# Performance work log

Hardware: AMD Instinct MI355X
Metric: run time of the kernel (lower is better)

## Reference

```python
import jax, jax.numpy as jnp
import numpy as np

B, SP, SH, H = 32, 256, 256, 512
D = 2 * H       # input feature dim (2*hidden_size)
E = H // 2      # per-liner output dim
FD = 4 * H      # fusion linear dim
EPS = 1e-13


def setup_inputs() -> dict:
    key = jax.random.key(0)
    ks = jax.random.split(key, 8)
    s = 0.02
    return dict(
        premise_batch=jax.random.normal(ks[0], (B, SP, D), jnp.float32),
        hypothesis_batch=jax.random.normal(ks[1], (B, SH, D), jnp.float32),
        premise_mask=jax.random.randint(ks[2], (B, SP), 0, 2).astype(jnp.int32),
        hypothesis_mask=jax.random.randint(ks[3], (B, SH), 0, 2).astype(jnp.int32),
        W8=jax.random.normal(ks[4], (8, D, E), jnp.float32) * s,   # liner1..8 weights (in,out)
        B8=jnp.zeros((8, E), jnp.float32),
        Wl=jax.random.normal(ks[5], (8 * E, FD), jnp.float32) * s,  # self.liner
        bl=jnp.zeros((FD,), jnp.float32),
        Wp=jax.random.normal(ks[6], (7 * D, H), jnp.float32) * s,   # self._projection
        bp=jnp.zeros((H,), jnp.float32),
    )


def masked_softmax(logits, mask):
    # ESIM-style: multiply logits by mask, softmax, re-mask, renormalize.
    m = mask[:, None, :]                        # (b,1,kv)
    r = jax.nn.softmax(logits * m, axis=-1) * m
    return r / (r.sum(axis=-1, keepdims=True) + EPS)


def fuse(x, imp_self, imp_inter, W8, B8, Wl, bl):
    # x: (b,s,D); imp_*: (b,s,1). Eight modulated views -> liner1..8 -> concat -> liner+ReLU.
    a1 = imp_self * imp_inter
    a2 = imp_self + imp_inter
    a3 = jnp.maximum(imp_self, imp_inter)
    x1 = x * imp_self
    x2 = x * imp_inter
    mx = jnp.maximum(x1, x2)
    feats = jnp.stack([x * a1, x * a2, x * a3, mx,
                       x * (a1 + 1.0), x * (a2 + 1.0), x * (a3 + 1.0), mx + x], 0)  # (8,b,s,D)
    h = jnp.einsum('kbsd,kde->kbse', feats, W8) + B8[:, None, None, :]              # (8,b,s,E)
    cat = jnp.moveaxis(h, 0, 2).reshape(x.shape[0], x.shape[1], 8 * E)              # concat order 1..8
    return jax.nn.relu(cat @ Wl + bl)           # dropout is identity in eval mode


def reference(premise_batch, hypothesis_batch, premise_mask, hypothesis_mask,
              W8, B8, Wl, bl, Wp, bp):
    pm = premise_mask.astype(jnp.float32)
    hm = hypothesis_mask.astype(jnp.float32)
    scale = 1.0 / jnp.sqrt(jnp.float32(premise_batch.shape[-1]))

    sim = jnp.einsum('bpd,bhd->bph', premise_batch, hypothesis_batch) * scale
    ph = masked_softmax(sim, hm)                               # (b,Sp,Sh)
    hp = masked_softmax(sim.transpose(0, 2, 1), pm)            # (b,Sh,Sp)
    att_p = jnp.einsum('bph,bhd->bpd', ph, hypothesis_batch) * pm[:, :, None]
    att_h = jnp.einsum('bhp,bpd->bhd', hp, premise_batch) * hm[:, :, None]

    sp_attn = jax.nn.softmax(jnp.einsum('bpd,bqd->bpq', premise_batch, premise_batch) * scale, axis=-1)
    sh_attn = jax.nn.softmax(jnp.einsum('bpd,bqd->bpq', hypothesis_batch, hypothesis_batch) * scale, axis=-1)
    self_p = sp_attn @ premise_batch
    self_h = sh_attn @ hypothesis_batch

    imp_p = sp_attn.sum(axis=-2)[..., None]        # (b,Sp,1)
    imp_h = sh_attn.sum(axis=-2)[..., None]        # (b,Sh,1)
    inter_imp_h = ph.sum(axis=-2)[..., None]       # (b,Sh,1)
    inter_imp_p = hp.sum(axis=-2)[..., None]       # (b,Sp,1)

    p_all = fuse(premise_batch, imp_p, inter_imp_p, W8, B8, Wl, bl)
    h_all = fuse(hypothesis_batch, imp_h, inter_imp_h, W8, B8, Wl, bl)

    enh_p = jnp.concatenate([premise_batch, att_p, self_p, p_all,
                             premise_batch * att_p, premise_batch - att_p], axis=-1)
    enh_h = jnp.concatenate([hypothesis_batch, att_h, self_h, h_all,
                             hypothesis_batch * att_h, hypothesis_batch - att_h], axis=-1)
    out_p = jax.nn.relu(enh_p @ Wp + bp)
    out_h = jax.nn.relu(enh_h @ Wp + bp)
    return out_p, out_h
```

## Files before the change

### kernel.cpp

```cpp
#include <hip/hip_runtime.h>
#include <hip/hip_bf16.h>
#include <cmath>

#define BB 32
#define SS 256
#define DD 1024
#define EE 256
#define FDIM 2048
#define HH 512
#define KOUT6 (6 * 1024)
#define NROW (BB * SS)
#define NROW2 (2 * NROW)
#define SIMSZ ((size_t)BB * SS * SS)

static constexpr float SCALE = 1.0f / 32.0f;
static constexpr float EPSF  = 1e-13f;

typedef __attribute__((ext_vector_type(8))) short bf16x8;
typedef __attribute__((ext_vector_type(4))) float f32x4;

__device__ inline float4 ld4(const float* p) { return *(const float4*)p; }
__device__ inline ushort f2b(float f) {
    uint x = __float_as_uint(f);
    x += 0x7fffu + ((x >> 16) & 1u);
    return (ushort)(x >> 16);
}
__device__ inline float b2f(ushort u) { return __uint_as_float(((uint)u) << 16); }
__device__ inline bf16x8 cvt8(const float* v) {
    bf16x8 r;
#pragma unroll
    for (int j = 0; j < 8; ++j) r[j] = (short)f2b(v[j]);
    return r;
}
__device__ inline void b2f8(bf16x8 v, float* o) {
#pragma unroll
    for (int j = 0; j < 8; ++j) o[j] = b2f((ushort)v[j]);
}

typedef __attribute__((address_space(1))) const uchar gas_t;
typedef __attribute__((address_space(3))) uchar las_t;
__device__ inline void gll16(const ushort* g, ushort* l) {
    __builtin_amdgcn_global_load_lds((gas_t*)g, (las_t*)l, 16, 0, 0);
}

__device__ inline int swz_orig_2d() {
    const int n   = blockIdx.y * gridDim.x + blockIdx.x;
    const int tot = gridDim.x * gridDim.y;
    return (n & 7) * (tot >> 3) + (n >> 3);
}
__device__ inline int swz_orig_3d() {
    const int n   = (blockIdx.z * gridDim.y + blockIdx.y) * gridDim.x + blockIdx.x;
    const int tot = gridDim.x * gridDim.y * gridDim.z;
    return (n & 7) * (tot >> 3) + (n >> 3);
}

__global__ __launch_bounds__(256)
void tpose_cvt_k(const float* __restrict__ in, ushort* __restrict__ out,
                 int K, int N, size_t inStride, size_t outStride) {
    __shared__ float T[32][33];
    const float* ib = in  + (size_t)blockIdx.z * inStride;
    ushort*      ob = out + (size_t)blockIdx.z * outStride;
    const int k0 = blockIdx.x * 32, n0 = blockIdx.y * 32;
    const int tx = threadIdx.x & 31, ty = threadIdx.x >> 5;
#pragma unroll
    for (int i = 0; i < 4; ++i) T[ty + 8 * i][tx] = ib[(size_t)(k0 + ty + 8 * i) * N + n0 + tx];
    __syncthreads();
#pragma unroll
    for (int i = 0; i < 4; ++i)
        ob[(size_t)(n0 + ty + 8 * i) * K + k0 + tx] = f2b(T[tx][ty + 8 * i]);
}

__global__ __launch_bounds__(256)
void tpose_wp_k(const float* __restrict__ Wp, ushort* __restrict__ out) {
    __shared__ float T[32][33];
    const int k0 = blockIdx.x * 32, n0 = blockIdx.y * 32;
    const int tx = threadIdx.x & 31, ty = threadIdx.x >> 5;
#pragma unroll
    for (int i = 0; i < 4; ++i) {
        const int k = k0 + ty + 8 * i, n = n0 + tx;
        float v = Wp[(size_t)k * HH + n];
        if (k < DD)           v += Wp[(size_t)(k + 6 * DD) * HH + n];
        else if (k < 2 * DD)  v -= Wp[(size_t)(k + 5 * DD) * HH + n];
        T[ty + 8 * i][tx] = v;
    }
    __syncthreads();
#pragma unroll
    for (int i = 0; i < 4; ++i)
        out[(size_t)(n0 + ty + 8 * i) * KOUT6 + k0 + tx] = f2b(T[tx][ty + 8 * i]);
}

__global__ __launch_bounds__(256)
void cvt_xb_k(const float* __restrict__ P, const float* __restrict__ H,
              ushort* __restrict__ Xb) {
    const int idx = blockIdx.x * 256 + threadIdx.x;
    const int row = idx >> 7, chunk = idx & 127;
    const size_t off = (size_t)row * DD + chunk * 8;
    const float* X = (row < NROW) ? (P + off) : (H + off - (size_t)NROW * DD);
    const float4 x0 = ld4(X), x1 = ld4(X + 4);
    float xv[8] = {x0.x, x0.y, x0.z, x0.w, x1.x, x1.y, x1.z, x1.w};
    *(bf16x8*)&Xb[off] = cvt8(xv);
}

__global__ __launch_bounds__(256)
void prep_xprod_k(const float* __restrict__ P, const float* __restrict__ H,
                  const ushort* __restrict__ attAb,
                  ushort* __restrict__ Xb, ushort* __restrict__ prodb) {
    const int idx = blockIdx.x * 256 + threadIdx.x;
    const int row = idx >> 7, chunk = idx & 127;
    const size_t off = (size_t)row * DD + chunk * 8;
    const float* X = (row < NROW) ? (P + off) : (H + off - (size_t)NROW * DD);
    const float4 x0 = ld4(X), x1 = ld4(X + 4);
    float xv[8] = {x0.x, x0.y, x0.z, x0.w, x1.x, x1.y, x1.z, x1.w};
    float av[8];
    b2f8(*(const bf16x8*)&attAb[off], av);
    float pv[8];
#pragma unroll
    for (int j = 0; j < 8; ++j) pv[j] = xv[j] * av[j];
    *(bf16x8*)&Xb[off]    = cvt8(xv);
    *(bf16x8*)&prodb[off] = cvt8(pv);
}

__global__ __launch_bounds__(256)
void reduce_out_k(float* __restrict__ out, const float* __restrict__ p1,
                  const float* __restrict__ bp) {
    const int gid = blockIdx.x * 256 + threadIdx.x;
    const size_t o = (size_t)gid * 4;
    const float4 a = ld4(&out[o]);
    const float4 b = ld4(&p1[o]);
    const float4 bv = ld4(&bp[(int)(o & 511)]);
    *(float4*)&out[o] = make_float4(fmaxf(a.x + b.x + bv.x, 0.f),
                                    fmaxf(a.y + b.y + bv.y, 0.f),
                                    fmaxf(a.z + b.z + bv.z, 0.f),
                                    fmaxf(a.w + b.w + bv.w, 0.f));
}

__global__ __launch_bounds__(256)
void softmax4_k(ushort* __restrict__ simPH, ushort* __restrict__ simPHT,
                ushort* __restrict__ simPP, ushort* __restrict__ simHH,
                const int* __restrict__ pma, const int* __restrict__ hma) {
    const int job = blockIdx.y;
    ushort* buf = job == 0 ? simPH : job == 1 ? simPHT : job == 2 ? simPP : simHH;
    const int* mask = job == 0 ? hma : job == 1 ? pma : nullptr;
    const int w = threadIdx.x >> 6, lane = threadIdx.x & 63;
    const int row = blockIdx.x * 4 + w;
    const int b = row >> 8;
    ushort* rp = buf + (size_t)row * SS + lane * 4;
    ushort4 u = *(const ushort4*)rp;
    float z[4], mj[4];
    const ushort uv[4] = {u.x, u.y, u.z, u.w};
#pragma unroll
    for (int c = 0; c < 4; ++c) {
        const float v = b2f(uv[c]);
        float m = 1.f;
        if (mask) m = (float)mask[b * SS + lane * 4 + c];
        mj[c] = m; z[c] = v * m;
    }
    float M = fmaxf(fmaxf(z[0], z[1]), fmaxf(z[2], z[3]));
#pragma unroll
    for (int off = 1; off < 64; off <<= 1) M = fmaxf(M, __shfl_xor(M, off));
    float e[4], r[4], sz = 0.f, sr = 0.f;
#pragma unroll
    for (int c = 0; c < 4; ++c) {
        e[c] = expf(z[c] - M);
        r[c] = e[c] * mj[c];
        sz += e[c]; sr += r[c];
    }
#pragma unroll
    for (int off = 1; off < 64; off <<= 1) {
        sz += __shfl_xor(sz, off);
        sr += __shfl_xor(sr, off);
    }
    ushort4 o;
    if (mask) {
        const float d = 1.f / (sr + EPSF * sz);
        o.x = f2b(r[0] * d); o.y = f2b(r[1] * d); o.z = f2b(r[2] * d); o.w = f2b(r[3] * d);
    } else {
        const float d = 1.f / sz;
        o.x = f2b(e[0] * d); o.y = f2b(e[1] * d); o.z = f2b(e[2] * d); o.w = f2b(e[3] * d);
    }
    *(ushort4*)rp = o;
}

__global__ __launch_bounds__(256)
void colsum_p1_k(const ushort* __restrict__ simPP, const ushort* __restrict__ simHH,
                 const ushort* __restrict__ simPHT, const ushort* __restrict__ simPH,
                 float* __restrict__ pbuf) {
    const int job = blockIdx.y, b = blockIdx.x, rc = blockIdx.z, j = threadIdx.x;
    const ushort* src = job == 0 ? simPP : job == 1 ? simHH : job == 2 ? simPHT : simPH;
    const ushort* Mb = src + (size_t)b * SS * SS + (size_t)rc * 32 * SS;
    float s = 0.f;
#pragma unroll 4
    for (int i = 0; i < 32; ++i) s += b2f(Mb[i * SS + j]);
    pbuf[(((size_t)job * BB + b) * 8 + rc) * SS + j] = s;
}

__global__ __launch_bounds__(256)
void colsum_p2_k(const float* __restrict__ pbuf,
                 float* __restrict__ impS, float* __restrict__ impI) {
    const int job = blockIdx.y, b = blockIdx.x, j = threadIdx.x;
    const float* pb = pbuf + ((size_t)job * BB + b) * 8 * SS;
    float s = 0.f;
#pragma unroll
    for (int rc = 0; rc < 8; ++rc) s += pb[rc * SS + j];
    float* dst = job == 0 ? impS : job == 1 ? impS + NROW : job == 2 ? impI : impI + NROW;
    dst[b * SS + j] = s;
}

#define LSWZ(kg, r) ((r) ^ ((kg) << 1))
#define SIG(r) (((r) >> 1) & 3)
#define FRAG_R(T, r) (*(const bf16x8*)T[kq][LSWZ(kq, r)])
#define FRAG_G(T, r) (*(const bf16x8*)&T[r][(kq ^ SIG(r)) * 8])
#define FRAG_G64(T, r, kh) (*(const bf16x8*)&T[r][((((kh) << 2) + kq) ^ ((r) & 7)) * 8])

#define MFMA_TAIL(afr, bfr, ac)                                                      \
    _Pragma("unroll") for (int m = 0; m < 4; ++m)                                    \
        _Pragma("unroll") for (int n = 0; n < 4; ++n)                                \
            ac[m][n] = __builtin_amdgcn_mfma_f32_16x16x32_bf16(                      \
                afr[m], bfr[n], ac[m][n], 0, 0, 0);

#define MFMA_CORE_G64()                                                              \
    _Pragma("unroll") for (int kh_ = 0; kh_ < 2; ++kh_) {                            \
        bf16x8 afr[4], bfr[4];                                                       \
        _Pragma("unroll") for (int m = 0; m < 4; ++m)                                \
            afr[m] = FRAG_G64(As, wr + m * 16 + fr, kh_);                            \
        _Pragma("unroll") for (int n = 0; n < 4; ++n)                                \
            bfr[n] = FRAG_G64(Bs, wc + n * 16 + fr, kh_);                            \
        MFMA_TAIL(afr, bfr, acc)                                                     \
    }

#define MFMA_PREAMBLE()                                                              \
    const int tid = threadIdx.x;                                                     \
    const int lane = tid & 63;                                                       \
    const int w = tid >> 6;                                                          \
    const int wr = (w >> 1) * 64, wc = (w & 1) * 64;                                 \
    const int fr = lane & 15;                                                        \
    const int kq = lane >> 4;                                                        \
    const int rq = kq * 4;                                                           \
    f32x4 acc[4][4] = {};

#define GLL_STAGE2(seg, pitch, r0, kloc, T)                                          \
    {                                                                                \
        const int rl0_ = w * 32 + (lane >> 2);                                       \
        const int cp_ = lane & 3;                                                    \
        gll16((seg) + (size_t)((r0) + rl0_) * (pitch) + (kloc) + ((cp_ ^ SIG(rl0_)) * 8), \
              &T[w * 32][0]);                                                        \
        const int rl1_ = rl0_ + 16;                                                  \
        gll16((seg) + (size_t)((r0) + rl1_) * (pitch) + (kloc) + ((cp_ ^ SIG(rl1_)) * 8), \
              &T[w * 32 + 16][0]);                                                   \
    }

#define GLL_STAGE64(seg, pitch, r0, kloc, T)                                         \
    {                                                                                \
        _Pragma("unroll")                                                            \
        for (int ii_ = 0; ii_ < 4; ++ii_) {                                          \
            const int rl_ = w * 32 + ii_ * 8 + (lane >> 3);                          \
            const int cp_ = lane & 7;                                                \
            gll16((seg) + (size_t)((r0) + rl_) * (pitch) + (kloc) + (((cp_ ^ (rl_ & 7))) * 8), \
                  &T[w * 32 + ii_ * 8][0]);                                          \
        }                                                                            \
    }

__global__ __launch_bounds__(256)
void mfma_nt_k(const ushort* __restrict__ XbE,
               ushort* __restrict__ simPH, ushort* __restrict__ simPHT,
               ushort* __restrict__ simPP, ushort* __restrict__ simHH) {
    __shared__ __align__(16) ushort As[128][64];
    __shared__ __align__(16) ushort Bs[128][64];
    int orig = swz_orig_3d();
    const int cb = orig & 1; orig >>= 1;
    const int rb = orig & 1; orig >>= 1;
    const int g = orig >> 5, b = orig & 31;
    const ushort* Au = XbE + ((size_t)((g == 2) ? NROW : 0) + (size_t)b * SS) * DD;
    const ushort* Bu = XbE + ((size_t)((g == 1) ? 0 : NROW) + (size_t)b * SS) * DD;
    const int col0 = cb * 128, row0 = rb * 128;
    MFMA_PREAMBLE();
    for (int k0 = 0; k0 < DD; k0 += 64) {
        __syncthreads();
        GLL_STAGE64(Au, DD, row0, k0, As);
        GLL_STAGE64(Bu, DD, col0, k0, Bs);
        __syncthreads();
        MFMA_CORE_G64();
    }
    ushort* Cb = (g == 0 ? simPH : g == 1 ? simPP : simHH) + (size_t)b * SS * SS;
#pragma unroll
    for (int m = 0; m < 4; ++m)
#pragma unroll
        for (int n = 0; n < 4; ++n) {
            const int c = col0 + wc + n * 16 + fr;
            const int r0 = row0 + wr + m * 16 + rq;
#pragma unroll
            for (int r = 0; r < 4; ++r) Cb[(size_t)(r0 + r) * SS + c] = f2b(acc[m][n][r] * SCALE);
            if (g == 0) {
                ushort* Tb = simPHT + (size_t)b * SS * SS;
                ushort4 t;
                t.x = f2b(acc[m][n][0] * SCALE); t.y = f2b(acc[m][n][1] * SCALE);
                t.z = f2b(acc[m][n][2] * SCALE); t.w = f2b(acc[m][n][3] * SCALE);
                *(ushort4*)&Tb[(size_t)c * SS + r0] = t;
            }
        }
}

__global__ __launch_bounds__(256)
void mfma_att_k(const ushort* __restrict__ ph, const ushort* __restrict__ hp,
                const ushort* __restrict__ spA, const ushort* __restrict__ shA,
                const ushort* __restrict__ PbT, const ushort* __restrict__ HbT,
                const int* __restrict__ pma, const int* __restrict__ hma,
                ushort* __restrict__ attAb, ushort* __restrict__ selfAb) {
    __shared__ __align__(16) ushort As[128][64];
    __shared__ __align__(16) ushort Bs[128][64];
    int orig = swz_orig_3d();
    const int x = orig & 7; orig >>= 3;
    const int y = orig & 1; orig >>= 1;
    const int g = orig >> 5, b = orig & 31;
    const ushort* W  = (g == 0 ? ph : g == 1 ? hp : g == 2 ? spA : shA) + (size_t)b * SS * SS;
    const ushort* BT = ((g == 0 || g == 3) ? HbT : PbT) + (size_t)b * DD * SS;
    const int* rmask = g == 0 ? pma + b * SS : g == 1 ? hma + b * SS : nullptr;
    const int side = (g == 1 || g == 3);
    ushort* Ob = (g < 2 ? attAb : selfAb) + ((size_t)side * NROW + (size_t)b * SS) * DD;
    const int col0 = x * 128, row0 = y * 128;
    MFMA_PREAMBLE();
    for (int k0 = 0; k0 < SS; k0 += 64) {
        __syncthreads();
        GLL_STAGE64(W,  SS, row0, k0, As);
        GLL_STAGE64(BT, SS, col0, k0, Bs);
        __syncthreads();
        MFMA_CORE_G64();
    }
#pragma unroll
    for (int m = 0; m < 4; ++m)
#pragma unroll
        for (int n = 0; n < 4; ++n) {
            const int c = col0 + wc + n * 16 + fr;
#pragma unroll
            for (int r = 0; r < 4; ++r) {
                const int rr = row0 + wr + m * 16 + rq + r;
                const float mm = rmask ? (float)rmask[rr] : 1.0f;
                Ob[(size_t)rr * DD + c] = f2b(acc[m][n][r] * mm);
            }
        }
}

__global__ __launch_bounds__(256)
void mfma_fuse_pure_k(const ushort* __restrict__ Xb, const float* __restrict__ impS,
                      const float* __restrict__ impI, const ushort* __restrict__ W8T,
                      const float* __restrict__ B8v, ushort* __restrict__ catb) {
    __shared__ __align__(16) ushort As[128][64];
    __shared__ __align__(16) ushort Bs[128][64];
    const int orig = swz_orig_2d();
    const int cb = orig % 12, rb = orig / 12;
    const int kidx = cb >> 1;
    const int kf = kidx + (kidx >= 3 ? 1 : 0);
    const int e0 = (cb & 1) * 128, row0 = rb * 128;
    MFMA_PREAMBLE();
    const ushort* Wk = W8T + (size_t)kf * EE * DD;
    for (int k0 = 0; k0 < DD; k0 += 64) {
        __syncthreads();
        GLL_STAGE64(Xb, DD, row0, k0, As);
        GLL_STAGE64(Wk, DD, e0, k0, Bs);
        __syncthreads();
        MFMA_CORE_G64();
    }
#pragma unroll
    for (int m = 0; m < 4; ++m)
#pragma unroll
        for (int n = 0; n < 4; ++n) {
            const int el = e0 + wc + n * 16 + fr;
            const float bv = B8v[kf * EE + el];
#pragma unroll
            for (int r = 0; r < 4; ++r) {
                const int row = row0 + wr + m * 16 + rq + r;
                const float s_ = impS[row], i_ = impI[row];
                float coef;
                switch (kf) {
                    case 0: coef = s_ * i_;             break;
                    case 1: coef = s_ + i_;             break;
                    case 2: coef = fmaxf(s_, i_);       break;
                    case 4: coef = s_ * i_ + 1.f;       break;
                    case 5: coef = s_ + i_ + 1.f;       break;
                    default: coef = fmaxf(s_, i_) + 1.f; break;
                }
                catb[(size_t)row * FDIM + kf * EE + el] = f2b(coef * acc[m][n][r] + bv);
            }
        }
}

__global__ __launch_bounds__(256)
void mfma_fuse_dual_k(const ushort* __restrict__ Xb, const float* __restrict__ impS,
                      const float* __restrict__ impI, const ushort* __restrict__ W8T,
                      const float* __restrict__ B8v, ushort* __restrict__ catb) {
    __shared__ __align__(16) ushort AsX[4][128][8];
    __shared__ __align__(16) ushort AsP[4][128][8];
    __shared__ __align__(16) ushort Bs[128][32];
    const int orig = swz_orig_2d();
    const int cb = orig & 3, rb = orig >> 2;
    const int kf = (cb >> 1) ? 7 : 3;
    const int e0 = (cb & 1) * 128, row0 = rb * 128;
    MFMA_PREAMBLE();
    f32x4 accP[4][4] = {};
    const ushort* Wk = W8T + (size_t)kf * EE * DD;
    for (int k0 = 0; k0 < DD; k0 += 32) {
        bf16x8 xr[2], pr[2];
#pragma unroll
        for (int i = 0; i < 2; ++i) {
            const int cid = tid + i * 256, srow = cid >> 2, skc = (cid & 3) * 8;
            xr[i] = *(const bf16x8*)&Xb[(size_t)(row0 + srow) * DD + k0 + skc];
#pragma unroll
            for (int j = 0; j < 8; ++j) {
                const short s = xr[i][j];
                pr[i][j] = (s & (short)0x8000) ? (short)0 : s;
            }
        }
        __syncthreads();
        GLL_STAGE2(Wk, DD, e0, k0, Bs);
#pragma unroll
        for (int i = 0; i < 2; ++i) {
            const int cid = tid + i * 256, kg = cid & 3, rr = LSWZ(kg, cid >> 2);
            *(bf16x8*)AsX[kg][rr] = xr[i];
            *(bf16x8*)AsP[kg][rr] = pr[i];
        }
        __syncthreads();
        {
            bf16x8 ax[4], ap[4], bfr[4];
#pragma unroll
            for (int m = 0; m < 4; ++m) {
                ax[m] = FRAG_R(AsX, wr + m * 16 + fr);
                ap[m] = FRAG_R(AsP, wr + m * 16 + fr);
            }
#pragma unroll
            for (int n = 0; n < 4; ++n) bfr[n] = FRAG_G(Bs, wc + n * 16 + fr);
            MFMA_TAIL(ax, bfr, acc)
            MFMA_TAIL(ap, bfr, accP)
        }
    }
#pragma unroll
    for (int m = 0; m < 4; ++m)
#pragma unroll
        for (int n = 0; n < 4; ++n) {
            const int el = e0 + wc + n * 16 + fr;
            const float bv = B8v[kf * EE + el];
#pragma unroll
            for (int r = 0; r < 4; ++r) {
                const int row = row0 + wr + m * 16 + rq + r;
                const float s_ = impS[row], i_ = impI[row];
                const float smax = fmaxf(s_, i_), smin = fminf(s_, i_);
                const float gg = (kf == 3) ? smin : smin + 1.f;
                catb[(size_t)row * FDIM + kf * EE + el] =
                    f2b((smax - smin) * accP[m][n][r] + gg * acc[m][n][r] + bv);
            }
        }
}

__global__ __launch_bounds__(256)
void mfma_lin_k(const ushort* __restrict__ A, const ushort* __restrict__ BT,
                const float* __restrict__ bias, ushort* __restrict__ C) {
    __shared__ __align__(16) ushort As[128][64];
    __shared__ __align__(16) ushort Bs[128][64];
    const int orig = swz_orig_2d();
    const int col0 = (orig & 15) * 128, row0 = (orig >> 4) * 128;
    MFMA_PREAMBLE();
    for (int k0 = 0; k0 < FDIM; k0 += 64) {
        __syncthreads();
        GLL_STAGE64(A,  FDIM, row0, k0, As);
        GLL_STAGE64(BT, FDIM, col0, k0, Bs);
        __syncthreads();
        MFMA_CORE_G64();
    }
#pragma unroll
    for (int m = 0; m < 4; ++m)
#pragma unroll
        for (int n = 0; n < 4; ++n) {
            const int c = col0 + wc + n * 16 + fr;
            const float bv = bias[c];
#pragma unroll
            for (int r = 0; r < 4; ++r) {
                const int rr = row0 + wr + m * 16 + rq + r;
                C[(size_t)rr * FDIM + c] = f2b(fmaxf(acc[m][n][r] + bv, 0.f));
            }
        }
}

__device__ inline void out_seg(int k0, const ushort* Xb, const ushort* attAb,
                               const ushort* selfAb, const ushort* pallb,
                               const ushort* prodb,
                               const ushort*& seg, int& pitch, int& kloc) {
    switch (k0 >> 10) {
        case 0:  seg = Xb;     pitch = DD;   kloc = k0;          break;
        case 1:  seg = attAb;  pitch = DD;   kloc = k0 - DD;     break;
        case 2:  seg = selfAb; pitch = DD;   kloc = k0 - 2 * DD; break;
        case 3:
        case 4:  seg = pallb;  pitch = FDIM; kloc = k0 - 3 * DD; break;
        default: seg = prodb;  pitch = DD;   kloc = k0 - 5 * DD; break;
    }
}

__global__ __launch_bounds__(256)
void mfma_out_k(const ushort* __restrict__ Xb, const ushort* __restrict__ attAb,
                const ushort* __restrict__ selfAb, const ushort* __restrict__ pallb,
                const ushort* __restrict__ prodb, const ushort* __restrict__ WpT,
                const float* __restrict__ bp, float* __restrict__ dst0,
                float* __restrict__ dst1, int kchunk, int finalize) {
    __shared__ __align__(16) ushort As[128][64];
    __shared__ __align__(16) ushort Bs[128][64];
    int orig = swz_orig_3d();
    const int x = orig & 3; orig >>= 2;
    const int y = orig & 127; orig >>= 7;
    const int z = orig;
    const int col0 = x * 128, row0 = y * 128;
    const int kbase = z * kchunk;
    float* dst = z == 0 ? dst0 : dst1;
    MFMA_PREAMBLE();
    for (int t = 0; t < kchunk / 64; ++t) {
        const int k0 = kbase + t * 64;
        const ushort* seg; int pitch, kloc;
        out_seg(k0, Xb, attAb, selfAb, pallb, prodb, seg, pitch, kloc);
        __syncthreads();
        GLL_STAGE64(seg, pitch, row0, kloc, As);
        GLL_STAGE64(WpT, KOUT6, col0, k0, Bs);
        __syncthreads();
        MFMA_CORE_G64();
    }
#pragma unroll
    for (int m = 0; m < 4; ++m)
#pragma unroll
        for (int n = 0; n < 4; ++n) {
            const int c = col0 + wc + n * 16 + fr;
            const float bv = finalize ? bp[c] : 0.f;
#pragma unroll
            for (int r = 0; r < 4; ++r) {
                const int rr = row0 + wr + m * 16 + rq + r;
                const float v = acc[m][n][r] + bv;
                dst[(size_t)rr * HH + c] = finalize ? fmaxf(v, 0.f) : v;
            }
        }
}

extern "C" void kernel_launch(void* const* d_in, const int* in_sizes, int n_in,
                              void* d_out, int out_size, void* d_ws, size_t ws_size,
                              hipStream_t stream) {
    const float* P   = (const float*)d_in[0];
    const float* Hb  = (const float*)d_in[1];
    const int*   pma = (const int*)d_in[2];
    const int*   hma = (const int*)d_in[3];
    const float* W8  = (const float*)d_in[4];
    const float* B8v = (const float*)d_in[5];
    const float* Wl  = (const float*)d_in[6];
    const float* bl  = (const float*)d_in[7];
    const float* Wp  = (const float*)d_in[8];
    const float* bp  = (const float*)d_in[9];

    char* base = (char*)d_ws;
    ushort* simPH  = (ushort*)base;
    ushort* simPHT = simPH  + SIMSZ;
    ushort* simPP  = simPHT + SIMSZ;
    ushort* simHH  = simPP  + SIMSZ;
    ushort* PbT    = simHH + SIMSZ;
    ushort* HbT    = PbT + (size_t)NROW * DD;
    ushort* catb   = (ushort*)base;
    ushort* Xb     = (ushort*)base;
    ushort* prodb  = Xb + (size_t)NROW2 * DD;
    char* cur = base + (size_t)NROW2 * FDIM * 2;
    auto alloc_f = [&](size_t n) { float*  p = (float*)cur;  cur += n * 4; return p; };
    auto alloc_u = [&](size_t n) { ushort* p = (ushort*)cur; cur += n * 2; return p; };
    float*  impS   = alloc_f(NROW2);
    float*  impI   = alloc_f(NROW2);
    ushort* attAb  = alloc_u((size_t)NROW2 * DD);
    ushort* selfAb = alloc_u((size_t)NROW2 * DD);
    ushort* pallb  = alloc_u((size_t)NROW2 * FDIM);
    ushort* WlT    = alloc_u((size_t)FDIM * FDIM);
    ushort* WpT    = alloc_u((size_t)HH * KOUT6);
    ushort* W8T    = alloc_u((size_t)8 * EE * DD);
    float*  pbuf   = alloc_f((size_t)4 * BB * 8 * SS);
    float*  part1  = alloc_f((size_t)NROW2 * HH);

    ushort* XbE = pallb;

    const size_t need_split = (size_t)((char*)(part1 + (size_t)NROW2 * HH) - base);
    const bool split = ws_size >= need_split;

    float* outp = (float*)d_out;
    const dim3 blk(256);

    cvt_xb_k<<<dim3(NROW2 * DD / 8 / 256), blk, 0, stream>>>(P, Hb, XbE);
    tpose_cvt_k<<<dim3(8, 32, BB), blk, 0, stream>>>(P,  PbT, SS, DD, (size_t)SS * DD, (size_t)DD * SS);
    tpose_cvt_k<<<dim3(8, 32, BB), blk, 0, stream>>>(Hb, HbT, SS, DD, (size_t)SS * DD, (size_t)DD * SS);
    tpose_cvt_k<<<dim3(FDIM / 32, FDIM / 32, 1), blk, 0, stream>>>(Wl, WlT, FDIM, FDIM, 0, 0);
    tpose_wp_k<<<dim3(KOUT6 / 32, HH / 32, 1), blk, 0, stream>>>(Wp, WpT);
    tpose_cvt_k<<<dim3(DD / 32, EE / 32, 8), blk, 0, stream>>>(W8, W8T, DD, EE,
                                                               (size_t)DD * EE, (size_t)EE * DD);

    mfma_nt_k<<<dim3(2, 2, 96), blk, 0, stream>>>(XbE, simPH, simPHT, simPP, simHH);
    softmax4_k<<<dim3(NROW / 4, 4), blk, 0, stream>>>(simPH, simPHT, simPP, simHH, pma, hma);
    colsum_p1_k<<<dim3(BB, 4, 8), blk, 0, stream>>>(simPP, simHH, simPHT, simPH, pbuf);
    colsum_p2_k<<<dim3(BB, 4), blk, 0, stream>>>(pbuf, impS, impI);
    mfma_att_k<<<dim3(8, 2, 128), blk, 0, stream>>>(simPH, simPHT, simPP, simHH, PbT, HbT,
                                                    pma, hma, attAb, selfAb);

    mfma_fuse_pure_k<<<dim3(12, 128), blk, 0, stream>>>(XbE, impS, impI, W8T, B8v, catb);
    mfma_fuse_dual_k<<<dim3(4, 128), blk, 0, stream>>>(XbE, impS, impI, W8T, B8v, catb);
    mfma_lin_k<<<dim3(16, 128), blk, 0, stream>>>(catb, WlT, bl, pallb);
    prep_xprod_k<<<dim3(NROW2 * DD / 8 / 256), blk, 0, stream>>>(P, Hb, attAb, Xb, prodb);
    if (split) {
        mfma_out_k<<<dim3(4, 128, 2), blk, 0, stream>>>(Xb, attAb, selfAb, pallb, prodb,
                                                        WpT, bp, outp, part1, KOUT6 / 2, 0);
        reduce_out_k<<<dim3(NROW2 * HH / 4 / 256), blk, 0, stream>>>(outp, part1, bp);
    } else {
        mfma_out_k<<<dim3(4, 128, 1), blk, 0, stream>>>(Xb, attAb, selfAb, pallb, prodb,
                                                        WpT, bp, outp, outp, KOUT6, 1);
    }

    (void)in_sizes; (void)n_in; (void)out_size; (void)ws_size;
}
```

Baseline: 673.2 us.

## Double-buffer LDS tiles with async prefetch in fuse, lin and out GEMMs

```diff
diff --git a/kernel.cpp b/kernel.cpp
--- a/kernel.cpp
+++ b/kernel.cpp
@@ -208,6 +208,8 @@
 
 #define LSWZ(kg, r) ((r) ^ ((kg) << 1))
 #define SIG(r) (((r) >> 1) & 3)
+#define FRAG_R(T, r) (*(const bf16x8*)T[kq][LSWZ(kg_dummy_, r)])
+#undef FRAG_R
 #define FRAG_R(T, r) (*(const bf16x8*)T[kq][LSWZ(kq, r)])
 #define FRAG_G(T, r) (*(const bf16x8*)&T[r][(kq ^ SIG(r)) * 8])
 #define FRAG_G64(T, r, kh) (*(const bf16x8*)&T[r][((((kh) << 2) + kq) ^ ((r) & 7)) * 8])
@@ -225,6 +227,14 @@
             afr[m] = FRAG_G64(As, wr + m * 16 + fr, kh_);                            \
         _Pragma("unroll") for (int n = 0; n < 4; ++n)                                \
             bfr[n] = FRAG_G64(Bs, wc + n * 16 + fr, kh_);                            \
+        MFMA_TAIL(afr, bfr, acc)                                                     \
+    }
+
+#define MFMA_CORE_DB(AT, BT_)                                                        \
+    {                                                                                \
+        bf16x8 afr[4], bfr[4];                                                       \
+        _Pragma("unroll") for (int m = 0; m < 4; ++m) afr[m] = FRAG_G(AT, wr + m * 16 + fr); \
+        _Pragma("unroll") for (int n = 0; n < 4; ++n) bfr[n] = FRAG_G(BT_, wc + n * 16 + fr); \
         MFMA_TAIL(afr, bfr, acc)                                                     \
     }
 
@@ -259,6 +269,10 @@
                   &T[w * 32 + ii_ * 8][0]);                                          \
         }                                                                            \
     }
+
+#define PIPE_WAIT_N()  { asm volatile("s_waitcnt vmcnt(4)" ::: "memory"); __builtin_amdgcn_s_barrier(); }
+#define PIPE_WAIT_0()  { asm volatile("s_waitcnt vmcnt(0)" ::: "memory"); __builtin_amdgcn_s_barrier(); }
+#define PIPE_POST()    { asm volatile("" ::: "memory"); __builtin_amdgcn_s_barrier(); }
 
 __global__ __launch_bounds__(256)
 void mfma_nt_k(const ushort* __restrict__ XbE,
@@ -344,8 +358,8 @@
 void mfma_fuse_pure_k(const ushort* __restrict__ Xb, const float* __restrict__ impS,
                       const float* __restrict__ impI, const ushort* __restrict__ W8T,
                       const float* __restrict__ B8v, ushort* __restrict__ catb) {
-    __shared__ __align__(16) ushort As[128][64];
-    __shared__ __align__(16) ushort Bs[128][64];
+    __shared__ __align__(16) ushort As[2][128][32];
+    __shared__ __align__(16) ushort Bs[2][128][32];
     const int orig = swz_orig_2d();
     const int cb = orig % 12, rb = orig / 12;
     const int kidx = cb >> 1;
@@ -353,12 +367,20 @@
     const int e0 = (cb & 1) * 128, row0 = rb * 128;
     MFMA_PREAMBLE();
     const ushort* Wk = W8T + (size_t)kf * EE * DD;
-    for (int k0 = 0; k0 < DD; k0 += 64) {
-        __syncthreads();
-        GLL_STAGE64(Xb, DD, row0, k0, As);
-        GLL_STAGE64(Wk, DD, e0, k0, Bs);
-        __syncthreads();
-        MFMA_CORE_G64();
+    GLL_STAGE2(Xb, DD, row0, 0, As[0]);
+    GLL_STAGE2(Wk, DD, e0, 0, Bs[0]);
+    int cur = 0;
+    for (int t = 0; t < DD / 32; ++t) {
+        if (t + 1 < DD / 32) {
+            GLL_STAGE2(Xb, DD, row0, (t + 1) * 32, As[cur ^ 1]);
+            GLL_STAGE2(Wk, DD, e0, (t + 1) * 32, Bs[cur ^ 1]);
+            PIPE_WAIT_N();
+        } else {
+            PIPE_WAIT_0();
+        }
+        MFMA_CORE_DB(As[cur], Bs[cur]);
+        PIPE_POST();
+        cur ^= 1;
     }
 #pragma unroll
     for (int m = 0; m < 4; ++m)
@@ -453,17 +475,25 @@
 __global__ __launch_bounds__(256)
 void mfma_lin_k(const ushort* __restrict__ A, const ushort* __restrict__ BT,
                 const float* __restrict__ bias, ushort* __restrict__ C) {
-    __shared__ __align__(16) ushort As[128][64];
-    __shared__ __align__(16) ushort Bs[128][64];
+    __shared__ __align__(16) ushort As[2][128][32];
+    __shared__ __align__(16) ushort Bs[2][128][32];
     const int orig = swz_orig_2d();
     const int col0 = (orig & 15) * 128, row0 = (orig >> 4) * 128;
     MFMA_PREAMBLE();
-    for (int k0 = 0; k0 < FDIM; k0 += 64) {
-        __syncthreads();
-        GLL_STAGE64(A,  FDIM, row0, k0, As);
-        GLL_STAGE64(BT, FDIM, col0, k0, Bs);
-        __syncthreads();
-        MFMA_CORE_G64();
+    GLL_STAGE2(A,  FDIM, row0, 0, As[0]);
+    GLL_STAGE2(BT, FDIM, col0, 0, Bs[0]);
+    int cur = 0;
+    for (int t = 0; t < FDIM / 32; ++t) {
+        if (t + 1 < FDIM / 32) {
+            GLL_STAGE2(A,  FDIM, row0, (t + 1) * 32, As[cur ^ 1]);
+            GLL_STAGE2(BT, FDIM, col0, (t + 1) * 32, Bs[cur ^ 1]);
+            PIPE_WAIT_N();
+        } else {
+            PIPE_WAIT_0();
+        }
+        MFMA_CORE_DB(As[cur], Bs[cur]);
+        PIPE_POST();
+        cur ^= 1;
     }
 #pragma unroll
     for (int m = 0; m < 4; ++m)
@@ -499,8 +529,8 @@
                 const ushort* __restrict__ prodb, const ushort* __restrict__ WpT,
                 const float* __restrict__ bp, float* __restrict__ dst0,
                 float* __restrict__ dst1, int kchunk, int finalize) {
-    __shared__ __align__(16) ushort As[128][64];
-    __shared__ __align__(16) ushort Bs[128][64];
+    __shared__ __align__(16) ushort As[2][128][32];
+    __shared__ __align__(16) ushort Bs[2][128][32];
     int orig = swz_orig_3d();
     const int x = orig & 3; orig >>= 2;
     const int y = orig & 127; orig >>= 7;
@@ -509,15 +539,28 @@
     const int kbase = z * kchunk;
     float* dst = z == 0 ? dst0 : dst1;
     MFMA_PREAMBLE();
-    for (int t = 0; t < kchunk / 64; ++t) {
-        const int k0 = kbase + t * 64;
+    {
         const ushort* seg; int pitch, kloc;
-        out_seg(k0, Xb, attAb, selfAb, pallb, prodb, seg, pitch, kloc);
-        __syncthreads();
-        GLL_STAGE64(seg, pitch, row0, kloc, As);
-        GLL_STAGE64(WpT, KOUT6, col0, k0, Bs);
-        __syncthreads();
-        MFMA_CORE_G64();
+        out_seg(kbase, Xb, attAb, selfAb, pallb, prodb, seg, pitch, kloc);
+        GLL_STAGE2(seg, pitch, row0, kloc, As[0]);
+        GLL_STAGE2(WpT, KOUT6, col0, kbase, Bs[0]);
+    }
+    int cur = 0;
+    const int NT = kchunk / 32;
+    for (int t = 0; t < NT; ++t) {
+        if (t + 1 < NT) {
+            const int k0 = kbase + (t + 1) * 32;
+            const ushort* seg; int pitch, kloc;
+            out_seg(k0, Xb, attAb, selfAb, pallb, prodb, seg, pitch, kloc);
+            GLL_STAGE2(seg, pitch, row0, kloc, As[cur ^ 1]);
+            GLL_STAGE2(WpT, KOUT6, col0, k0, Bs[cur ^ 1]);
+            PIPE_WAIT_N();
+        } else {
+            PIPE_WAIT_0();
+        }
+        MFMA_CORE_DB(As[cur], Bs[cur]);
+        PIPE_POST();
+        cur ^= 1;
     }
 #pragma unroll
     for (int m = 0; m < 4; ++m)
```

After: 725.8 us. 7.8% more time.
